# Kernel tuning notes

Measured on AMD Instinct MI355X. Metric: run time of the kernel, lower is better.

The kernel has to match this reference:

```python
import jax, jax.numpy as jnp
import numpy as np
from jax import lax

B, N, T, NX = 4, 512, 24, 8
H = 64
PRED_LEN, NY = 12, 1
E_RAND = 8192
EPS = 1e-5


def setup_inputs() -> dict:
    key = jax.random.key(0)
    ks = jax.random.split(key, 24)
    sc = lambda k, shape: (jax.random.normal(k, shape, jnp.float32) * 0.05)
    x = jax.random.normal(ks[0], (B, N, T, NX), jnp.float32)
    er = jax.random.randint(ks[1], (2, E_RAND), 0, N, dtype=jnp.int32)
    loops = jnp.stack([jnp.arange(N, dtype=jnp.int32), jnp.arange(N, dtype=jnp.int32)])
    edge_index = jnp.concatenate([er, loops], axis=1)  # [2, 8704]
    return {
        'x': x,
        'edge_index': edge_index,
        'W_fc': sc(ks[2], (NX, H)), 'b_fc': jnp.zeros((H,), jnp.float32),
        'W1': sc(ks[3], (H, H)), 'a_l1': sc(ks[4], (H,)), 'a_r1': sc(ks[5], (H,)), 'bias1': jnp.zeros((H,), jnp.float32),
        'W2': sc(ks[6], (H, H)), 'a_l2': sc(ks[7], (H,)), 'a_r2': sc(ks[8], (H,)), 'bias2': jnp.zeros((H,), jnp.float32),
        'W_ih': sc(ks[9], (4 * H, H)), 'W_hh': sc(ks[10], (4 * H, H)),
        'b_ih': jnp.zeros((4 * H,), jnp.float32), 'b_hh': jnp.zeros((4 * H,), jnp.float32),
        'g_l': jnp.ones((H,), jnp.float32), 'b_l': jnp.zeros((H,), jnp.float32),
        'g_g': jnp.ones((H,), jnp.float32), 'b_g': jnp.zeros((H,), jnp.float32),
        'W_d': sc(ks[11], (H, PRED_LEN * NY)), 'b_d': jnp.zeros((PRED_LEN * NY,), jnp.float32),
    }


def _layer_norm(x, g, b):
    mu = jnp.mean(x, axis=-1, keepdims=True)
    var = jnp.mean(jnp.square(x - mu), axis=-1, keepdims=True)
    return (x - mu) * lax.rsqrt(var + EPS) * g + b


def _gat(x, W, a_l, a_r, bias, mask):
    # x: [B,N,T,F] -> operate in [B,T,N,H] layout (torch transpose(1,2))
    h = jnp.einsum('bntf,fh->btnh', x, W)          # [B,T,N,H]
    el = jnp.einsum('btnh,h->btn', h, a_l)          # attn_l
    er = jnp.einsum('btnh,h->btn', h, a_r)          # attn_r
    e = el[..., :, None] + er[..., None, :]         # [B,T,N,N]
    e = jax.nn.leaky_relu(e, negative_slope=0.2)
    e = jnp.where(mask, e, -jnp.inf)
    alpha = jax.nn.softmax(e, axis=-1)
    out = jnp.einsum('btmn,btnh->bmth', alpha, h) + bias  # back to [B,N,T,H]
    return jax.nn.gelu(out, approximate=False)


def _lstm(xseq, W_ih, W_hh, b_ih, b_hh):
    # xseq: [M, T, H] -> outputs [M, T, H]; PyTorch gate order i,f,g,o
    M = xseq.shape[0]
    Hh = W_hh.shape[1]
    b = b_ih + b_hh
    def step(carry, xt):
        hprev, cprev = carry
        gates = xt @ W_ih.T + hprev @ W_hh.T + b
        i, f, g, o = jnp.split(gates, 4, axis=-1)
        c = jax.nn.sigmoid(f) * cprev + jax.nn.sigmoid(i) * jnp.tanh(g)
        h = jax.nn.sigmoid(o) * jnp.tanh(c)
        return (h, c), h
    init = (jnp.zeros((M, Hh), xseq.dtype), jnp.zeros((M, Hh), xseq.dtype))
    _, hs = lax.scan(step, init, xseq.transpose(1, 0, 2))  # [T,M,H]
    return hs.transpose(1, 0, 2)


def reference(x, edge_index, W_fc, b_fc, W1, a_l1, a_r1, bias1, W2, a_l2, a_r2, bias2,
              W_ih, W_hh, b_ih, b_hh, g_l, b_l, g_g, b_g, W_d, b_d):
    Bb, Nn, Tt, _ = x.shape
    mask = jnp.zeros((Nn, Nn), bool).at[edge_index[0], edge_index[1]].set(True)
    x_h = jnp.einsum('bntf,fh->bnth', x, W_fc) + b_fc          # fc
    g1 = _gat(x_h, W1, a_l1, a_r1, bias1, mask)                # conv1
    g2 = _gat(g1, W2, a_l2, a_r2, bias2, mask)                 # conv2
    l = _lstm(x_h.reshape(Bb * Nn, Tt, -1), W_ih, W_hh, b_ih, b_hh).reshape(Bb, Nn, Tt, -1)
    h = _layer_norm(g2, g_g, b_g) + _layer_norm(l, g_l, b_l)
    last = h[:, :, -1, :]                                       # [B,N,H]
    out = last @ W_d + b_d                                      # [B,N,pred_len*ny]
    return out.reshape(Bb, Nn, PRED_LEN, NY)
```

## Files before the change

### kernel.cpp

```cpp
#include <hip/hip_runtime.h>
#include <hip/hip_bf16.h>
#include <math.h>

#define BB 4
#define NN 512
#define TT 24
#define NXF 8
#define HH 64
#define PRED 12
#define MM (BB*NN)

typedef __attribute__((ext_vector_type(8))) short short8;
typedef __attribute__((ext_vector_type(4))) float f32x4;
typedef unsigned short ushort;

#define WS_HBUF    0
#define WS_H2      131072
#define WS_HL      262144
#define WS_EL      393216
#define WS_ER      395264
#define WS_EL2     397312
#define WS_ER2     399360
#define WS_WCOMB   401408
#define WS_BCOMB   403456
#define WS_WHHFRAG 403712

__device__ inline float sigm(float x){ return 1.f/(1.f+__expf(-x)); }
__device__ inline float tanh_fast(float x){ float e=__expf(2.f*x); return 1.f - 2.f/(e+1.f); }
__device__ inline float gelu_exact(float x){ return 0.5f*x*(1.f+erff(x*0.70710678118654752440f)); }
__device__ inline ushort f2bu(float f){
    unsigned b=__float_as_uint(f);
    return (ushort)((b + 0x7FFFu + ((b>>16)&1u))>>16);
}
__device__ inline float bu2f(ushort u){ return __uint_as_float(((unsigned)u)<<16); }

__device__ inline void split8(const float* f, short8& hi, short8& lo){
    #pragma unroll
    for (int j = 0; j < 8; ++j){
        ushort h = f2bu(f[j]);
        hi[j] = (short)h;
        lo[j] = (short)f2bu(f[j] - bu2f(h));
    }
}

__global__ __launch_bounds__(256,2) void gat1pre_kernel(
    const float* __restrict__ x, const float* __restrict__ Wfc, const float* __restrict__ bfc,
    const float* __restrict__ W1, const float* __restrict__ al1, const float* __restrict__ ar1,
    const float* __restrict__ Wih, const float* __restrict__ Whh,
    const float* __restrict__ bih, const float* __restrict__ bhh,
    float* __restrict__ Hbuf, float* __restrict__ el, float* __restrict__ er,
    float* __restrict__ wcombG, float* __restrict__ bcombG,
    ushort* __restrict__ whhfrag)
{
    __shared__ float sw1[HH*HH];
    __shared__ float swfc[NXF*HH];
    __shared__ float sb[HH], sal[HH], sar[HH];
    __shared__ float sxh[4][68];
    __shared__ float sx[4][NXF];
    const int t = threadIdx.x;

    if (blockIdx.x >= 512){
        const int f = blockIdx.x - 512;
        const int ng = t;
        float accf = 0.f, accb = 0.f;
        const float* wr = Wih + ng*64;
        #pragma unroll
        for (int k = 0; k < 64; ++k){
            float wv = wr[k];
            accf += Wfc[f*64 + k] * wv;
            accb += bfc[k] * wv;
        }
        wcombG[f*256 + ng] = accf;
        if (f == 0) bcombG[ng] = accb + bih[ng] + bhh[ng];
        #pragma unroll
        for (int u = 0; u < 8; ++u){
            int o = f*2048 + u*256 + t;
            int F  = o >> 9;
            int ln = (o >> 3) & 63;
            int j  = o & 7;
            int w_ = F >> 3, tt = (F >> 1) & 3, ks = F & 1;
            int q = ln >> 4, c = ln & 15;
            int ngx = (w_ + 4*tt)*16 + c;
            whhfrag[o] = f2bu(Whh[ngx*64 + ks*32 + q*8 + j]);
        }
        return;
    }

    const int r = t >> 6, h = t & 63;
    #pragma unroll
    for (int i = 0; i < 16; ++i) sw1[t + 256*i] = W1[t + 256*i];
    swfc[t] = Wfc[t];
    swfc[t+256] = Wfc[t+256];
    if (t < 64) sb[t] = bfc[t];
    else if (t < 128) sal[t-64] = al1[t-64];
    else if (t < 192) sar[t-128] = ar1[t-128];
    if (t < 32){
        int rr = t >> 3, f = t & 7;
        sx[rr][f] = x[(size_t)(blockIdx.x*4 + rr)*(TT*NXF) + (TT-1)*NXF + f];
    }
    __syncthreads();
    float xh = sb[h];
    #pragma unroll
    for (int f = 0; f < NXF; ++f) xh += sx[r][f]*swfc[f*HH + h];
    sxh[r][h] = xh;
    __syncthreads();
    float acc = 0.f;
    const float4* xr = (const float4*)&sxh[r][0];
    #pragma unroll
    for (int k4 = 0; k4 < 16; ++k4){
        float4 xv = xr[k4];
        acc += xv.x*sw1[(4*k4+0)*HH+h] + xv.y*sw1[(4*k4+1)*HH+h]
             + xv.z*sw1[(4*k4+2)*HH+h] + xv.w*sw1[(4*k4+3)*HH+h];
    }
    const int m = blockIdx.x*4 + r;
    Hbuf[(size_t)m*HH + h] = acc;
    float v1 = acc*sal[h], v2 = acc*sar[h];
    #pragma unroll
    for (int o = 32; o; o >>= 1){ v1 += __shfl_xor(v1,o); v2 += __shfl_xor(v2,o); }
    if (h == 0){ el[m] = v1; er[m] = v2; }
}

#define LHS 72
#define LXS 40
__global__ __launch_bounds__(256,2) void mid_fused_kernel(
    const float* __restrict__ Hbuf, const float* __restrict__ el_in, const float* __restrict__ er_in,
    const int* __restrict__ ei, int E,
    const float* __restrict__ bias1,
    const float* __restrict__ W2, const float* __restrict__ al2, const float* __restrict__ ar2,
    float* __restrict__ H2, float* __restrict__ el2, float* __restrict__ er2,
    const float* __restrict__ x,
    const float* __restrict__ wcombG, const float* __restrict__ bcombG,
    const ushort* __restrict__ whhfrag,
    float* __restrict__ hl)
{
    __shared__ __align__(16) char smem[58880];
    const int t = threadIdx.x;
    const int lane = t & 63;
    const int w = t >> 6;
    const int quad = lane >> 4;
    const int c16 = lane & 15;

    if (blockIdx.x >= 128){
        ushort* hbi = (ushort*)smem;
        ushort* hlo = (ushort*)(smem + 4608);
        ushort* xls = (ushort*)(smem + 9216);
        const int m0 = (blockIdx.x - 128) * 16;

        {
            unsigned* h0 = (unsigned*)hbi;
            unsigned* l0 = (unsigned*)hlo;
            for (int i = t; i < 2*16*LHS/2; i += 256){ h0[i] = 0u; l0[i] = 0u; }
            unsigned* xw = (unsigned*)xls;
            for (int i = t; i < TT*16*LXS/2; i += 256) xw[i] = 0u;
        }
        short8 bw[4][2]; short8 bx[4]; float bc[4];
        #pragma unroll
        for (int tt = 0; tt < 4; ++tt){
            const int ng = (w + 4*tt)*16 + c16;
            bc[tt] = bcombG[ng];
            #pragma unroll
            for (int ks = 0; ks < 2; ++ks)
                bw[tt][ks] = *(const short8*)&whhfrag[(((w*4+tt)*2)+ks)*512 + lane*8];
            short8 vx = {0,0,0,0,0,0,0,0};
            if (quad == 0){
                #pragma unroll
                for (int j = 0; j < 8; ++j) vx[j] = (short)f2bu(wcombG[j*256 + ng]);
            }
            bx[tt] = vx;
        }
        __syncthreads();
        for (int i = t; i < 16*TT*NXF; i += 256){
            int r = i / (TT*NXF);
            int rem = i - r*(TT*NXF);
            int st = rem >> 3, f = rem & 7;
            xls[st*(16*LXS) + r*LXS + f] = f2bu(x[(size_t)(m0+r)*(TT*NXF) + rem]);
        }
        __syncthreads();

        float cst[4] = {0,0,0,0};
        float hf[4]  = {0,0,0,0};

        for (int st = 0; st < TT; ++st){
            const int p = st & 1;
            const ushort* hb  = hbi + p*(16*LHS);
            const ushort* hl_ = hlo + p*(16*LHS);
            short8 ahi0 = *(const short8*)&hb[c16*LHS + quad*8];
            short8 ahi1 = *(const short8*)&hb[c16*LHS + 32 + quad*8];
            short8 alo0 = *(const short8*)&hl_[c16*LHS + quad*8];
            short8 alo1 = *(const short8*)&hl_[c16*LHS + 32 + quad*8];
            short8 ax   = *(const short8*)&xls[st*(16*LXS) + c16*LXS + quad*8];
            f32x4 acc[4];
            #pragma unroll
            for (int tt = 0; tt < 4; ++tt){
                f32x4 a = {bc[tt], bc[tt], bc[tt], bc[tt]};
                a = __builtin_amdgcn_mfma_f32_16x16x32_bf16(ax,   bx[tt],    a, 0,0,0);
                a = __builtin_amdgcn_mfma_f32_16x16x32_bf16(ahi0, bw[tt][0], a, 0,0,0);
                a = __builtin_amdgcn_mfma_f32_16x16x32_bf16(ahi1, bw[tt][1], a, 0,0,0);
                a = __builtin_amdgcn_mfma_f32_16x16x32_bf16(alo0, bw[tt][0], a, 0,0,0);
                a = __builtin_amdgcn_mfma_f32_16x16x32_bf16(alo1, bw[tt][1], a, 0,0,0);
                acc[tt] = a;
            }
            ushort* ho   = hbi + (p^1)*(16*LHS);
            ushort* lo_o = hlo + (p^1)*(16*LHS);
            #pragma unroll
            for (int reg = 0; reg < 4; ++reg){
                float gi = acc[0][reg], gf = acc[1][reg], gg = acc[2][reg], go = acc[3][reg];
                float cn = sigm(gf)*cst[reg] + sigm(gi)*tanh_fast(gg);
                cst[reg] = cn;
                float hn = sigm(go)*tanh_fast(cn);
                hf[reg] = hn;
                ushort hu = f2bu(hn);
                float lov = hn - bu2f(hu);
                int addr = (quad*4+reg)*LHS + w*16 + c16;
                ho[addr] = hu;
                lo_o[addr] = f2bu(lov);
            }
            __syncthreads();
        }
        #pragma unroll
        for (int reg = 0; reg < 4; ++reg)
            hl[(size_t)(m0 + quad*4 + reg)*HH + w*16 + c16] = hf[reg];
        return;
    }

    unsigned (*smask)[16] = (unsigned(*)[16])smem;
    float* er_s  = (float*)(smem + 1024);
    float* sal   = (float*)(smem + 3072);
    float* sar   = (float*)(smem + 3328);
    float (*alpha)[516] = (float(*)[516])(smem + 3584);
    float* uSpace = (float*)(smem + 36608);
    float (*xh2)[68] = (float(*)[68])(smem + 54528);

    const int b = blockIdx.x >> 5;
    const int m0 = (blockIdx.x & 31) * 16;
    const int l = lane;
    float (*HT)[70] = (float(*)[70])uSpace;

    if (t < 64) sal[t] = al2[t]; else if (t < 128) sar[t-64] = ar2[t-64];
    ((unsigned*)smask)[t] = 0;
    er_s[t] = er_in[b*NN + t];
    er_s[t+256] = er_in[b*NN + t + 256];
    __syncthreads();
    for (int e = t; e < E; e += 256){
        int s = ei[e];
        unsigned rl = (unsigned)(s - m0);
        if (rl < 16u){
            int d = ei[E + e];
            atomicOr(&smask[rl][d>>5], 1u << (d & 31));
        }
    }
    const float* Hbase = Hbuf + (size_t)b*NN*HH;
    const int nn = t >> 2, cc = t & 3;
    float4 r0,r1,r2,r3;
    {
        const float4* src = (const float4*)(Hbase + (size_t)nn*HH + cc*16);
        r0 = src[0]; r1 = src[1]; r2 = src[2]; r3 = src[3];
    }
    __syncthreads();
    for (int q = 0; q < 4; ++q){
        const int i = w*4 + q;
        const float elv = el_in[b*NN + m0 + i];
        float e8[8]; unsigned mk = 0; float mx = -1e30f;
        #pragma unroll
        for (int j = 0; j < 8; ++j){
            int n = l + 64*j;
            float ev = elv + er_s[n];
            ev = ev >= 0.f ? ev : 0.2f*ev;
            unsigned mb = (smask[i][(l>>5) + 2*j] >> (l & 31)) & 1u;
            e8[j] = ev;
            if (mb){ mk |= (1u<<j); mx = fmaxf(mx, ev); }
        }
        #pragma unroll
        for (int o = 32; o; o >>= 1) mx = fmaxf(mx, __shfl_xor(mx, o));
        float s = 0.f;
        #pragma unroll
        for (int j = 0; j < 8; ++j){
            float p = ((mk>>j) & 1u) ? __expf(e8[j]-mx) : 0.f;
            e8[j] = p; s += p;
        }
        #pragma unroll
        for (int o = 32; o; o >>= 1) s += __shfl_xor(s, o);
        const float inv = 1.f/s;
        #pragma unroll
        for (int j = 0; j < 8; ++j) alpha[i][l + 64*j] = e8[j]*inv;
    }
    __syncthreads();

    f32x4 acc = {0.f,0.f,0.f,0.f};
    for (int tile = 0; tile < 8; ++tile){
        {
            float v[16] = {r0.x,r0.y,r0.z,r0.w, r1.x,r1.y,r1.z,r1.w,
                           r2.x,r2.y,r2.z,r2.w, r3.x,r3.y,r3.z,r3.w};
            #pragma unroll
            for (int jj = 0; jj < 16; ++jj) HT[cc*16 + jj][nn] = v[jj];
        }
        if (tile < 7){
            const float4* src = (const float4*)(Hbase + (size_t)((tile+1)*64 + nn)*HH + cc*16);
            r0 = src[0]; r1 = src[1]; r2 = src[2]; r3 = src[3];
        }
        __syncthreads();
        #pragma unroll
        for (int ks = 0; ks < 2; ++ks){
            const int k0 = tile*64 + ks*32;
            const float* ap = &alpha[c16][k0 + quad*8];
            float4 a0 = *(const float4*)ap;
            float4 a1 = *(const float4*)(ap + 4);
            const float* bp = &HT[w*16 + c16][ks*32 + quad*8];
            float2 b0 = *(const float2*)bp,     b1 = *(const float2*)(bp+2);
            float2 b2 = *(const float2*)(bp+4), b3 = *(const float2*)(bp+6);
            float af[8] = {a0.x,a0.y,a0.z,a0.w,a1.x,a1.y,a1.z,a1.w};
            float bf[8] = {b0.x,b0.y,b1.x,b1.y,b2.x,b2.y,b3.x,b3.y};
            short8 ahi, alo, bhi, blo;
            split8(af, ahi, alo);
            split8(bf, bhi, blo);
            acc = __builtin_amdgcn_mfma_f32_16x16x32_bf16(ahi, bhi, acc, 0,0,0);
            acc = __builtin_amdgcn_mfma_f32_16x16x32_bf16(alo, bhi, acc, 0,0,0);
            acc = __builtin_amdgcn_mfma_f32_16x16x32_bf16(ahi, blo, acc, 0,0,0);
        }
        __syncthreads();
    }
    {
        const int h = w*16 + c16;
        const float bv = bias1[h];
        #pragma unroll
        for (int reg = 0; reg < 4; ++reg)
            xh2[quad*4 + reg][h] = gelu_exact(acc[reg] + bv);
    }
    __syncthreads();
    float* sw2 = uSpace;
    #pragma unroll
    for (int i = 0; i < 16; ++i) sw2[t + 256*i] = W2[t + 256*i];
    __syncthreads();
    {
        const int h = l;
        for (int q = 0; q < 4; ++q){
            const int i = w + 4*q;
            float acc2 = 0.f;
            const float4* xr = (const float4*)&xh2[i][0];
            #pragma unroll
            for (int k4 = 0; k4 < 16; ++k4){
                float4 xv = xr[k4];
                acc2 += xv.x*sw2[(4*k4+0)*HH+h] + xv.y*sw2[(4*k4+1)*HH+h]
                      + xv.z*sw2[(4*k4+2)*HH+h] + xv.w*sw2[(4*k4+3)*HH+h];
            }
            const int m = b*NN + m0 + i;
            H2[(size_t)m*HH + h] = acc2;
            float v1 = acc2*sal[h], v2 = acc2*sar[h];
            #pragma unroll
            for (int o = 32; o; o >>= 1){ v1 += __shfl_xor(v1,o); v2 += __shfl_xor(v2,o); }
            if (h == 0){ el2[m] = v1; er2[m] = v2; }
        }
    }
}

__global__ __launch_bounds__(256,2) void attn2_final_kernel(
    const float* __restrict__ Hbuf, const float* __restrict__ el_in, const float* __restrict__ er_in,
    const int* __restrict__ ei, int E,
    const float* __restrict__ bias2,
    const float* __restrict__ hl,
    const float* __restrict__ g_l, const float* __restrict__ b_l,
    const float* __restrict__ g_g, const float* __restrict__ b_g,
    const float* __restrict__ W_d, const float* __restrict__ b_d,
    float* __restrict__ out)
{
    __shared__ __align__(16) char smem[54016];
    unsigned (*smask)[16] = (unsigned(*)[16])smem;
    float* er_s  = (float*)(smem + 1024);
    float (*alpha)[516] = (float(*)[516])(smem + 3072);
    float* uSpace = (float*)(smem + 36096);

    const int t = threadIdx.x;
    const int b = blockIdx.x >> 5;
    const int m0 = (blockIdx.x & 31) * 16;
    const int l = t & 63, w = t >> 6;
    const int quad = l >> 4, c16 = l & 15;
    float (*HT)[70] = (float(*)[70])uSpace;

    ((unsigned*)smask)[t] = 0;
    er_s[t] = er_in[b*NN + t];
    er_s[t+256] = er_in[b*NN + t + 256];
    __syncthreads();
    for (int e = t; e < E; e += 256){
        int s = ei[e];
        unsigned rl = (unsigned)(s - m0);
        if (rl < 16u){
            int d = ei[E + e];
            atomicOr(&smask[rl][d>>5], 1u << (d & 31));
        }
    }
    const float* Hbase = Hbuf + (size_t)b*NN*HH;
    const int nn = t >> 2, cc = t & 3;
    float4 r0,r1,r2,r3;
    {
        const float4* src = (const float4*)(Hbase + (size_t)nn*HH + cc*16);
        r0 = src[0]; r1 = src[1]; r2 = src[2]; r3 = src[3];
    }
    __syncthreads();
    for (int q = 0; q < 4; ++q){
        const int i = w*4 + q;
        const float elv = el_in[b*NN + m0 + i];
        float e8[8]; unsigned mk = 0; float mx = -1e30f;
        #pragma unroll
        for (int j = 0; j < 8; ++j){
            int n = l + 64*j;
            float ev = elv + er_s[n];
            ev = ev >= 0.f ? ev : 0.2f*ev;
            unsigned mb = (smask[i][(l>>5) + 2*j] >> (l & 31)) & 1u;
            e8[j] = ev;
            if (mb){ mk |= (1u<<j); mx = fmaxf(mx, ev); }
        }
        #pragma unroll
        for (int o = 32; o; o >>= 1) mx = fmaxf(mx, __shfl_xor(mx, o));
        float s = 0.f;
        #pragma unroll
        for (int j = 0; j < 8; ++j){
            float p = ((mk>>j) & 1u) ? __expf(e8[j]-mx) : 0.f;
            e8[j] = p; s += p;
        }
        #pragma unroll
        for (int o = 32; o; o >>= 1) s += __shfl_xor(s, o);
        const float inv = 1.f/s;
        #pragma unroll
        for (int j = 0; j < 8; ++j) alpha[i][l + 64*j] = e8[j]*inv;
    }
    __syncthreads();

    f32x4 acc = {0.f,0.f,0.f,0.f};
    for (int tile = 0; tile < 8; ++tile){
        {
            float v[16] = {r0.x,r0.y,r0.z,r0.w, r1.x,r1.y,r1.z,r1.w,
                           r2.x,r2.y,r2.z,r2.w, r3.x,r3.y,r3.z,r3.w};
            #pragma unroll
            for (int jj = 0; jj < 16; ++jj) HT[cc*16 + jj][nn] = v[jj];
        }
        if (tile < 7){
            const float4* src = (const float4*)(Hbase + (size_t)((tile+1)*64 + nn)*HH + cc*16);
            r0 = src[0]; r1 = src[1]; r2 = src[2]; r3 = src[3];
        }
        __syncthreads();
        #pragma unroll
        for (int ks = 0; ks < 2; ++ks){
            const int k0 = tile*64 + ks*32;
            const float* ap = &alpha[c16][k0 + quad*8];
            float4 a0 = *(const float4*)ap;
            float4 a1 = *(const float4*)(ap + 4);
            const float* bp = &HT[w*16 + c16][ks*32 + quad*8];
            float2 b0 = *(const float2*)bp,     b1 = *(const float2*)(bp+2);
            float2 b2 = *(const float2*)(bp+4), b3 = *(const float2*)(bp+6);
            float af[8] = {a0.x,a0.y,a0.z,a0.w,a1.x,a1.y,a1.z,a1.w};
            float bf[8] = {b0.x,b0.y,b1.x,b1.y,b2.x,b2.y,b3.x,b3.y};
            short8 ahi, alo, bhi, blo;
            split8(af, ahi, alo);
            split8(bf, bhi, blo);
            acc = __builtin_amdgcn_mfma_f32_16x16x32_bf16(ahi, bhi, acc, 0,0,0);
            acc = __builtin_amdgcn_mfma_f32_16x16x32_bf16(alo, bhi, acc, 0,0,0);
            acc = __builtin_amdgcn_mfma_f32_16x16x32_bf16(ahi, blo, acc, 0,0,0);
        }
        __syncthreads();
    }
    float* sg2  = (float*)(smem + 3072);
    float* sdec = (float*)(smem + 36096);
    {
        const int h = w*16 + c16;
        const float bv = bias2[h];
        #pragma unroll
        for (int reg = 0; reg < 4; ++reg)
            sg2[(quad*4 + reg)*HH + h] = gelu_exact(acc[reg] + bv);
    }
    __syncthreads();
    const int gbase = b*NN + m0;
    {
        const int h = l;
        for (int q = 0; q < 4; ++q){
            const int ml = w*4 + q;
            float gv = sg2[ml*HH + h];
            float lv = hl[(size_t)(gbase + ml)*HH + h];

            float s1 = gv;
            #pragma unroll
            for (int o = 32; o; o >>= 1) s1 += __shfl_xor(s1, o);
            float dg = gv - s1*(1.f/64.f);
            float v1 = dg*dg;
            #pragma unroll
            for (int o = 32; o; o >>= 1) v1 += __shfl_xor(v1, o);
            float lng = dg*rsqrtf(v1*(1.f/64.f) + 1e-5f)*g_g[h] + b_g[h];

            float s2 = lv;
            #pragma unroll
            for (int o = 32; o; o >>= 1) s2 += __shfl_xor(s2, o);
            float dl = lv - s2*(1.f/64.f);
            float v2 = dl*dl;
            #pragma unroll
            for (int o = 32; o; o >>= 1) v2 += __shfl_xor(v2, o);
            float lnl = dl*rsqrtf(v2*(1.f/64.f) + 1e-5f)*g_l[h] + b_l[h];

            sdec[ml*HH + h] = lng + lnl;
        }
    }
    __syncthreads();
    if (t < 16*PRED){
        int rr = t / PRED, pp = t - rr*PRED;
        float a = b_d[pp];
        #pragma unroll
        for (int k = 0; k < HH; ++k) a += sdec[rr*HH + k]*W_d[k*PRED + pp];
        out[(size_t)(gbase + rr)*PRED + pp] = a;
    }
}

extern "C" void kernel_launch(void* const* d_in, const int* in_sizes, int n_in,
                              void* d_out, int out_size, void* d_ws, size_t ws_size,
                              hipStream_t stream){
    const float* x    = (const float*)d_in[0];
    const int*   ei   = (const int*)  d_in[1];
    const float* Wfc  = (const float*)d_in[2];
    const float* bfc  = (const float*)d_in[3];
    const float* W1   = (const float*)d_in[4];
    const float* al1  = (const float*)d_in[5];
    const float* ar1  = (const float*)d_in[6];
    const float* bias1= (const float*)d_in[7];
    const float* W2   = (const float*)d_in[8];
    const float* al2  = (const float*)d_in[9];
    const float* ar2  = (const float*)d_in[10];
    const float* bias2= (const float*)d_in[11];
    const float* Wih  = (const float*)d_in[12];
    const float* Whh  = (const float*)d_in[13];
    const float* bih  = (const float*)d_in[14];
    const float* bhh  = (const float*)d_in[15];
    const float* g_l  = (const float*)d_in[16];
    const float* b_l  = (const float*)d_in[17];
    const float* g_g  = (const float*)d_in[18];
    const float* b_g  = (const float*)d_in[19];
    const float* W_d  = (const float*)d_in[20];
    const float* b_d  = (const float*)d_in[21];

    float* ws = (float*)d_ws;
    const int E = in_sizes[1] / 2;

    gat1pre_kernel<<<512 + 8, 256, 0, stream>>>(x, Wfc, bfc, W1, al1, ar1,
                                                Wih, Whh, bih, bhh,
                                                ws+WS_HBUF, ws+WS_EL, ws+WS_ER,
                                                ws+WS_WCOMB, ws+WS_BCOMB,
                                                (ushort*)(ws+WS_WHHFRAG));
    mid_fused_kernel<<<256, 256, 0, stream>>>(ws+WS_HBUF, ws+WS_EL, ws+WS_ER,
                                              ei, E, bias1, W2, al2, ar2,
                                              ws+WS_H2, ws+WS_EL2, ws+WS_ER2,
                                              x, ws+WS_WCOMB, ws+WS_BCOMB,
                                              (const ushort*)(ws+WS_WHHFRAG),
                                              ws+WS_HL);
    attn2_final_kernel<<<BB*(NN/16), 256, 0, stream>>>(ws+WS_H2, ws+WS_EL2, ws+WS_ER2,
                                                       ei, E, bias2,
                                                       ws+WS_HL,
                                                       g_l, b_l, g_g, b_g, W_d, b_d,
                                                       (float*)d_out);
}
```

Before: 153.2 us.

## Precompute adjacency mask once and store H pre-split bf16 transposed

Adds an extra block to the first kernel that builds the full adjacency bitmask once in global memory, replacing the per-block edge scans with atomics in both attention kernels. The producers of H1 and H2 now write hi/lo bf16 halves in a feature-major transposed layout, so the aggregation loops read MFMA B fragments straight from global memory without the LDS transpose, tile syncs or per-iteration splitting. Alpha is split into hi/lo bf16 once in LDS, which shrinks shared memory. The cost is uncoalesced scattered 2-byte stores when writing the transposed H and a single block serially building the whole mask.

After: 152.7 us. No clear change (-0.3%).

```diff
diff --git a/kernel.cpp b/kernel.cpp
--- a/kernel.cpp
+++ b/kernel.cpp
@@ -14,16 +14,19 @@
 typedef __attribute__((ext_vector_type(4))) float f32x4;
 typedef unsigned short ushort;
 
-#define WS_HBUF    0
-#define WS_H2      131072
-#define WS_HL      262144
-#define WS_EL      393216
-#define WS_ER      395264
-#define WS_EL2     397312
-#define WS_ER2     399360
-#define WS_WCOMB   401408
-#define WS_BCOMB   403456
+#define WS_H1THI  0
+#define WS_H1TLO  65536
+#define WS_H2THI  131072
+#define WS_H2TLO  196608
+#define WS_HL     262144
+#define WS_EL     393216
+#define WS_ER     395264
+#define WS_EL2    397312
+#define WS_ER2    399360
+#define WS_WCOMB  401408
+#define WS_BCOMB  403456
 #define WS_WHHFRAG 403712
+#define WS_MASK   411904
 
 __device__ inline float sigm(float x){ return 1.f/(1.f+__expf(-x)); }
 __device__ inline float tanh_fast(float x){ float e=__expf(2.f*x); return 1.f - 2.f/(e+1.f); }
@@ -34,30 +37,37 @@
 }
 __device__ inline float bu2f(ushort u){ return __uint_as_float(((unsigned)u)<<16); }
 
-__device__ inline void split8(const float* f, short8& hi, short8& lo){
-    #pragma unroll
-    for (int j = 0; j < 8; ++j){
-        ushort h = f2bu(f[j]);
-        hi[j] = (short)h;
-        lo[j] = (short)f2bu(f[j] - bu2f(h));
-    }
-}
-
 __global__ __launch_bounds__(256,2) void gat1pre_kernel(
     const float* __restrict__ x, const float* __restrict__ Wfc, const float* __restrict__ bfc,
     const float* __restrict__ W1, const float* __restrict__ al1, const float* __restrict__ ar1,
     const float* __restrict__ Wih, const float* __restrict__ Whh,
     const float* __restrict__ bih, const float* __restrict__ bhh,
-    float* __restrict__ Hbuf, float* __restrict__ el, float* __restrict__ er,
+    const int* __restrict__ ei, int E,
+    ushort* __restrict__ H1Thi, ushort* __restrict__ H1Tlo,
+    float* __restrict__ el, float* __restrict__ er,
     float* __restrict__ wcombG, float* __restrict__ bcombG,
-    ushort* __restrict__ whhfrag)
+    ushort* __restrict__ whhfrag, unsigned* __restrict__ maskG)
 {
     __shared__ float sw1[HH*HH];
     __shared__ float swfc[NXF*HH];
     __shared__ float sb[HH], sal[HH], sar[HH];
     __shared__ float sxh[4][68];
     __shared__ float sx[4][NXF];
+    __shared__ unsigned msk[NN*16/2];
     const int t = threadIdx.x;
+
+    if (blockIdx.x >= 520){
+        for (int i = t; i < 8192; i += 256) msk[i] = 0u;
+        __syncthreads();
+        for (int e = t; e < E; e += 256){
+            int s = ei[e];
+            int d = ei[E + e];
+            atomicOr(&msk[s*16 + (d>>5)], 1u << (d & 31));
+        }
+        __syncthreads();
+        for (int i = t; i < 8192; i += 256) maskG[i] = msk[i];
+        return;
+    }
 
     if (blockIdx.x >= 512){
         const int f = blockIdx.x - 512;
@@ -113,7 +123,12 @@
              + xv.z*sw1[(4*k4+2)*HH+h] + xv.w*sw1[(4*k4+3)*HH+h];
     }
     const int m = blockIdx.x*4 + r;
-    Hbuf[(size_t)m*HH + h] = acc;
+    {
+        ushort hh = f2bu(acc);
+        size_t o = ((size_t)(m >> 9)*HH + h)*NN + (m & (NN-1));
+        H1Thi[o] = hh;
+        H1Tlo[o] = f2bu(acc - bu2f(hh));
+    }
     float v1 = acc*sal[h], v2 = acc*sar[h];
     #pragma unroll
     for (int o = 32; o; o >>= 1){ v1 += __shfl_xor(v1,o); v2 += __shfl_xor(v2,o); }
@@ -123,17 +138,19 @@
 #define LHS 72
 #define LXS 40
 __global__ __launch_bounds__(256,2) void mid_fused_kernel(
-    const float* __restrict__ Hbuf, const float* __restrict__ el_in, const float* __restrict__ er_in,
-    const int* __restrict__ ei, int E,
+    const ushort* __restrict__ H1Thi, const ushort* __restrict__ H1Tlo,
+    const float* __restrict__ el_in, const float* __restrict__ er_in,
+    const unsigned* __restrict__ maskG,
     const float* __restrict__ bias1,
     const float* __restrict__ W2, const float* __restrict__ al2, const float* __restrict__ ar2,
-    float* __restrict__ H2, float* __restrict__ el2, float* __restrict__ er2,
+    ushort* __restrict__ H2Thi, ushort* __restrict__ H2Tlo,
+    float* __restrict__ el2, float* __restrict__ er2,
     const float* __restrict__ x,
     const float* __restrict__ wcombG, const float* __restrict__ bcombG,
     const ushort* __restrict__ whhfrag,
     float* __restrict__ hl)
 {
-    __shared__ __align__(16) char smem[58880];
+    __shared__ __align__(16) char smem[41216];
     const int t = threadIdx.x;
     const int lane = t & 63;
     const int w = t >> 6;
@@ -227,35 +244,19 @@
     float* er_s  = (float*)(smem + 1024);
     float* sal   = (float*)(smem + 3072);
     float* sar   = (float*)(smem + 3328);
-    float (*alpha)[516] = (float(*)[516])(smem + 3584);
-    float* uSpace = (float*)(smem + 36608);
-    float (*xh2)[68] = (float(*)[68])(smem + 54528);
+    ushort (*ahi)[520] = (ushort(*)[520])(smem + 3584);
+    ushort (*alo_)[520] = (ushort(*)[520])(smem + 20224);
+    float (*xh2)[68] = (float(*)[68])(smem + 36864);
+    float* sw2 = (float*)(smem + 3584);
 
     const int b = blockIdx.x >> 5;
     const int m0 = (blockIdx.x & 31) * 16;
     const int l = lane;
-    float (*HT)[70] = (float(*)[70])uSpace;
 
     if (t < 64) sal[t] = al2[t]; else if (t < 128) sar[t-64] = ar2[t-64];
-    ((unsigned*)smask)[t] = 0;
+    ((unsigned*)smask)[t] = maskG[m0*16 + t];
     er_s[t] = er_in[b*NN + t];
     er_s[t+256] = er_in[b*NN + t + 256];
-    __syncthreads();
-    for (int e = t; e < E; e += 256){
-        int s = ei[e];
-        unsigned rl = (unsigned)(s - m0);
-        if (rl < 16u){
-            int d = ei[E + e];
-            atomicOr(&smask[rl][d>>5], 1u << (d & 31));
-        }
-    }
-    const float* Hbase = Hbuf + (size_t)b*NN*HH;
-    const int nn = t >> 2, cc = t & 3;
-    float4 r0,r1,r2,r3;
-    {
-        const float4* src = (const float4*)(Hbase + (size_t)nn*HH + cc*16);
-        r0 = src[0]; r1 = src[1]; r2 = src[2]; r3 = src[3];
-    }
     __syncthreads();
     for (int q = 0; q < 4; ++q){
         const int i = w*4 + q;
@@ -282,42 +283,31 @@
         for (int o = 32; o; o >>= 1) s += __shfl_xor(s, o);
         const float inv = 1.f/s;
         #pragma unroll
-        for (int j = 0; j < 8; ++j) alpha[i][l + 64*j] = e8[j]*inv;
+        for (int j = 0; j < 8; ++j){
+            float p = e8[j]*inv;
+            ushort ph = f2bu(p);
+            ahi[i][l + 64*j] = ph;
+            alo_[i][l + 64*j] = f2bu(p - bu2f(ph));
+        }
     }
     __syncthreads();
 
     f32x4 acc = {0.f,0.f,0.f,0.f};
-    for (int tile = 0; tile < 8; ++tile){
-        {
-            float v[16] = {r0.x,r0.y,r0.z,r0.w, r1.x,r1.y,r1.z,r1.w,
-                           r2.x,r2.y,r2.z,r2.w, r3.x,r3.y,r3.z,r3.w};
-            #pragma unroll
-            for (int jj = 0; jj < 16; ++jj) HT[cc*16 + jj][nn] = v[jj];
-        }
-        if (tile < 7){
-            const float4* src = (const float4*)(Hbase + (size_t)((tile+1)*64 + nn)*HH + cc*16);
-            r0 = src[0]; r1 = src[1]; r2 = src[2]; r3 = src[3];
-        }
-        __syncthreads();
-        #pragma unroll
-        for (int ks = 0; ks < 2; ++ks){
-            const int k0 = tile*64 + ks*32;
-            const float* ap = &alpha[c16][k0 + quad*8];
-            float4 a0 = *(const float4*)ap;
-            float4 a1 = *(const float4*)(ap + 4);
-            const float* bp = &HT[w*16 + c16][ks*32 + quad*8];
-            float2 b0 = *(const float2*)bp,     b1 = *(const float2*)(bp+2);
-            float2 b2 = *(const float2*)(bp+4), b3 = *(const float2*)(bp+6);
-            float af[8] = {a0.x,a0.y,a0.z,a0.w,a1.x,a1.y,a1.z,a1.w};
-            float bf[8] = {b0.x,b0.y,b1.x,b1.y,b2.x,b2.y,b3.x,b3.y};
-            short8 ahi, alo, bhi, blo;
-            split8(af, ahi, alo);
-            split8(bf, bhi, blo);
-            acc = __builtin_amdgcn_mfma_f32_16x16x32_bf16(ahi, bhi, acc, 0,0,0);
-            acc = __builtin_amdgcn_mfma_f32_16x16x32_bf16(alo, bhi, acc, 0,0,0);
-            acc = __builtin_amdgcn_mfma_f32_16x16x32_bf16(ahi, blo, acc, 0,0,0);
-        }
-        __syncthreads();
+    {
+        const ushort* bhiP = H1Thi + ((size_t)b*HH + w*16 + c16)*NN + quad*8;
+        const ushort* bloP = H1Tlo + ((size_t)b*HH + w*16 + c16)*NN + quad*8;
+        const ushort* ahiP = &ahi[c16][quad*8];
+        const ushort* aloP = &alo_[c16][quad*8];
+        #pragma unroll
+        for (int kk = 0; kk < 16; ++kk){
+            short8 fa_hi = *(const short8*)(ahiP + kk*32);
+            short8 fa_lo = *(const short8*)(aloP + kk*32);
+            short8 fb_hi = *(const short8*)(bhiP + kk*32);
+            short8 fb_lo = *(const short8*)(bloP + kk*32);
+            acc = __builtin_amdgcn_mfma_f32_16x16x32_bf16(fa_hi, fb_hi, acc, 0,0,0);
+            acc = __builtin_amdgcn_mfma_f32_16x16x32_bf16(fa_lo, fb_hi, acc, 0,0,0);
+            acc = __builtin_amdgcn_mfma_f32_16x16x32_bf16(fa_hi, fb_lo, acc, 0,0,0);
+        }
     }
     {
         const int h = w*16 + c16;
@@ -327,7 +317,6 @@
             xh2[quad*4 + reg][h] = gelu_exact(acc[reg] + bv);
     }
     __syncthreads();
-    float* sw2 = uSpace;
     #pragma unroll
     for (int i = 0; i < 16; ++i) sw2[t + 256*i] = W2[t + 256*i];
     __syncthreads();
@@ -343,19 +332,25 @@
                 acc2 += xv.x*sw2[(4*k4+0)*HH+h] + xv.y*sw2[(4*k4+1)*HH+h]
                       + xv.z*sw2[(4*k4+2)*HH+h] + xv.w*sw2[(4*k4+3)*HH+h];
             }
-            const int m = b*NN + m0 + i;
-            H2[(size_t)m*HH + h] = acc2;
+            const int m = m0 + i;
+            {
+                ushort vh = f2bu(acc2);
+                size_t o = ((size_t)b*HH + h)*NN + m;
+                H2Thi[o] = vh;
+                H2Tlo[o] = f2bu(acc2 - bu2f(vh));
+            }
             float v1 = acc2*sal[h], v2 = acc2*sar[h];
             #pragma unroll
             for (int o = 32; o; o >>= 1){ v1 += __shfl_xor(v1,o); v2 += __shfl_xor(v2,o); }
-            if (h == 0){ el2[m] = v1; er2[m] = v2; }
+            if (h == 0){ el2[b*NN + m] = v1; er2[b*NN + m] = v2; }
         }
     }
 }
 
 __global__ __launch_bounds__(256,2) void attn2_final_kernel(
-    const float* __restrict__ Hbuf, const float* __restrict__ el_in, const float* __restrict__ er_in,
-    const int* __restrict__ ei, int E,
+    const ushort* __restrict__ H2Thi, const ushort* __restrict__ H2Tlo,
+    const float* __restrict__ el_in, const float* __restrict__ er_in,
+    const unsigned* __restrict__ maskG,
     const float* __restrict__ bias2,
     const float* __restrict__ hl,
     const float* __restrict__ g_l, const float* __restrict__ b_l,
@@ -363,38 +358,23 @@
     const float* __restrict__ W_d, const float* __restrict__ b_d,
     float* __restrict__ out)
 {
-    __shared__ __align__(16) char smem[54016];
+    __shared__ __align__(16) char smem[40448];
     unsigned (*smask)[16] = (unsigned(*)[16])smem;
     float* er_s  = (float*)(smem + 1024);
-    float (*alpha)[516] = (float(*)[516])(smem + 3072);
-    float* uSpace = (float*)(smem + 36096);
+    ushort (*ahi)[520] = (ushort(*)[520])(smem + 3072);
+    ushort (*alo_)[520] = (ushort(*)[520])(smem + 19712);
+    float* sg2  = (float*)(smem + 36352);
+    float* sdec = (float*)(smem + 3072);
 
     const int t = threadIdx.x;
     const int b = blockIdx.x >> 5;
     const int m0 = (blockIdx.x & 31) * 16;
     const int l = t & 63, w = t >> 6;
     const int quad = l >> 4, c16 = l & 15;
-    float (*HT)[70] = (float(*)[70])uSpace;
-
-    ((unsigned*)smask)[t] = 0;
+
+    ((unsigned*)smask)[t] = maskG[m0*16 + t];
     er_s[t] = er_in[b*NN + t];
     er_s[t+256] = er_in[b*NN + t + 256];
-    __syncthreads();
-    for (int e = t; e < E; e += 256){
-        int s = ei[e];
-        unsigned rl = (unsigned)(s - m0);
-        if (rl < 16u){
-            int d = ei[E + e];
-            atomicOr(&smask[rl][d>>5], 1u << (d & 31));
-        }
-    }
-    const float* Hbase = Hbuf + (size_t)b*NN*HH;
-    const int nn = t >> 2, cc = t & 3;
-    float4 r0,r1,r2,r3;
-    {
-        const float4* src = (const float4*)(Hbase + (size_t)nn*HH + cc*16);
-        r0 = src[0]; r1 = src[1]; r2 = src[2]; r3 = src[3];
-    }
     __syncthreads();
     for (int q = 0; q < 4; ++q){
         const int i = w*4 + q;
@@ -421,45 +401,32 @@
         for (int o = 32; o; o >>= 1) s += __shfl_xor(s, o);
         const float inv = 1.f/s;
         #pragma unroll
-        for (int j = 0; j < 8; ++j) alpha[i][l + 64*j] = e8[j]*inv;
+        for (int j = 0; j < 8; ++j){
+            float p = e8[j]*inv;
+            ushort ph = f2bu(p);
+            ahi[i][l + 64*j] = ph;
+            alo_[i][l + 64*j] = f2bu(p - bu2f(ph));
+        }
     }
     __syncthreads();
 
     f32x4 acc = {0.f,0.f,0.f,0.f};
-    for (int tile = 0; tile < 8; ++tile){
-        {
-            float v[16] = {r0.x,r0.y,r0.z,r0.w, r1.x,r1.y,r1.z,r1.w,
-                           r2.x,r2.y,r2.z,r2.w, r3.x,r3.y,r3.z,r3.w};
-            #pragma unroll
-            for (int jj = 0; jj < 16; ++jj) HT[cc*16 + jj][nn] = v[jj];
-        }
-        if (tile < 7){
-            const float4* src = (const float4*)(Hbase + (size_t)((tile+1)*64 + nn)*HH + cc*16);
-            r0 = src[0]; r1 = src[1]; r2 = src[2]; r3 = src[3];
-        }
-        __syncthreads();
-        #pragma unroll
-        for (int ks = 0; ks < 2; ++ks){
-            const int k0 = tile*64 + ks*32;
-            const float* ap = &alpha[c16][k0 + quad*8];
-            float4 a0 = *(const float4*)ap;
-            float4 a1 = *(const float4*)(ap + 4);
-            const float* bp = &HT[w*16 + c16][ks*32 + quad*8];
-            float2 b0 = *(const float2*)bp,     b1 = *(const float2*)(bp+2);
-            float2 b2 = *(const float2*)(bp+4), b3 = *(const float2*)(bp+6);
-            float af[8] = {a0.x,a0.y,a0.z,a0.w,a1.x,a1.y,a1.z,a1.w};
-            float bf[8] = {b0.x,b0.y,b1.x,b1.y,b2.x,b2.y,b3.x,b3.y};
-            short8 ahi, alo, bhi, blo;
-            split8(af, ahi, alo);
-            split8(bf, bhi, blo);
-            acc = __builtin_amdgcn_mfma_f32_16x16x32_bf16(ahi, bhi, acc, 0,0,0);
-            acc = __builtin_amdgcn_mfma_f32_16x16x32_bf16(alo, bhi, acc, 0,0,0);
-            acc = __builtin_amdgcn_mfma_f32_16x16x32_bf16(ahi, blo, acc, 0,0,0);
-        }
-        __syncthreads();
-    }
-    float* sg2  = (float*)(smem + 3072);
-    float* sdec = (float*)(smem + 36096);
+    {
+        const ushort* bhiP = H2Thi + ((size_t)b*HH + w*16 + c16)*NN + quad*8;
+        const ushort* bloP = H2Tlo + ((size_t)b*HH + w*16 + c16)*NN + quad*8;
+        const ushort* ahiP = &ahi[c16][quad*8];
+        const ushort* aloP = &alo_[c16][quad*8];
+        #pragma unroll
+        for (int kk = 0; kk < 16; ++kk){
+            short8 fa_hi = *(const short8*)(ahiP + kk*32);
+            short8 fa_lo = *(const short8*)(aloP + kk*32);
+            short8 fb_hi = *(const short8*)(bhiP + kk*32);
+            short8 fb_lo = *(const short8*)(bloP + kk*32);
+            acc = __builtin_amdgcn_mfma_f32_16x16x32_bf16(fa_hi, fb_hi, acc, 0,0,0);
+            acc = __builtin_amdgcn_mfma_f32_16x16x32_bf16(fa_lo, fb_hi, acc, 0,0,0);
+            acc = __builtin_amdgcn_mfma_f32_16x16x32_bf16(fa_hi, fb_lo, acc, 0,0,0);
+        }
+    }
     {
         const int h = w*16 + c16;
         const float bv = bias2[h];
@@ -536,20 +503,27 @@
     float* ws = (float*)d_ws;
     const int E = in_sizes[1] / 2;
 
-    gat1pre_kernel<<<512 + 8, 256, 0, stream>>>(x, Wfc, bfc, W1, al1, ar1,
-                                                Wih, Whh, bih, bhh,
-                                                ws+WS_HBUF, ws+WS_EL, ws+WS_ER,
-                                                ws+WS_WCOMB, ws+WS_BCOMB,
-                                                (ushort*)(ws+WS_WHHFRAG));
-    mid_fused_kernel<<<256, 256, 0, stream>>>(ws+WS_HBUF, ws+WS_EL, ws+WS_ER,
-                                              ei, E, bias1, W2, al2, ar2,
-                                              ws+WS_H2, ws+WS_EL2, ws+WS_ER2,
+    gat1pre_kernel<<<521, 256, 0, stream>>>(x, Wfc, bfc, W1, al1, ar1,
+                                            Wih, Whh, bih, bhh,
+                                            ei, E,
+                                            (ushort*)(ws+WS_H1THI), (ushort*)(ws+WS_H1TLO),
+                                            ws+WS_EL, ws+WS_ER,
+                                            ws+WS_WCOMB, ws+WS_BCOMB,
+                                            (ushort*)(ws+WS_WHHFRAG),
+                                            (unsigned*)(ws+WS_MASK));
+    mid_fused_kernel<<<256, 256, 0, stream>>>((const ushort*)(ws+WS_H1THI), (const ushort*)(ws+WS_H1TLO),
+                                              ws+WS_EL, ws+WS_ER,
+                                              (const unsigned*)(ws+WS_MASK),
+                                              bias1, W2, al2, ar2,
+                                              (ushort*)(ws+WS_H2THI), (ushort*)(ws+WS_H2TLO),
+                                              ws+WS_EL2, ws+WS_ER2,
                                               x, ws+WS_WCOMB, ws+WS_BCOMB,
                                               (const ushort*)(ws+WS_WHHFRAG),
                                               ws+WS_HL);
-    attn2_final_kernel<<<BB*(NN/16), 256, 0, stream>>>(ws+WS_H2, ws+WS_EL2, ws+WS_ER2,
-                                                       ei, E, bias2,
-                                                       ws+WS_HL,
+    attn2_final_kernel<<<BB*(NN/16), 256, 0, stream>>>((const ushort*)(ws+WS_H2THI), (const ushort*)(ws+WS_H2TLO),
+                                                       ws+WS_EL2, ws+WS_ER2,
+                                                       (const unsigned*)(ws+WS_MASK),
+                                                       bias2, ws+WS_HL,
                                                        g_l, b_l, g_g, b_g, W_d, b_d,
                                                        (float*)d_out);
 }
```
